# Kernel tuning notes

Hardware: AMD Instinct MI355X
Metric: run time of the kernel (lower is better)

Reference implementation:

```python
import jax, jax.numpy as jnp
import numpy as np

B, NL, NH = 16, 4096, 1024
CL, CH = 128, 256
IN_CH, OUT_CH = CH + CL, 256  # 384 -> 256
BN_EPS = 1e-5
K = 3


def setup_inputs() -> dict:
    key = jax.random.key(0)
    ks = jax.random.split(key, 8)
    xyz_low = jax.random.normal(ks[0], (B, NL, 3), jnp.float32)
    xyz_high = jax.random.normal(ks[1], (B, NH, 3), jnp.float32)
    feat_low = jax.random.normal(ks[2], (B, CL, NL), jnp.float32)
    feat_high = jax.random.normal(ks[3], (B, CH, NH), jnp.float32)
    # Conv1d(kernel=1) params, kaiming-ish scale
    W = jax.random.normal(ks[4], (OUT_CH, IN_CH), jnp.float32) * (1.0 / np.sqrt(IN_CH))
    b = jax.random.normal(ks[5], (OUT_CH,), jnp.float32) * 0.01
    gamma = jnp.ones((OUT_CH,), jnp.float32)
    beta = jnp.zeros((OUT_CH,), jnp.float32)
    return {"xyz_low": xyz_low, "xyz_high": xyz_high, "feat_low": feat_low,
            "feat_high": feat_high, "W": W, "b": b, "gamma": gamma, "beta": beta}


def reference(xyz_low, xyz_high, feat_low, feat_high, W, b, gamma, beta):
    # --- three_nn: pairwise Euclidean distances (B, Nl, Nh), as torch.cdist ---
    sq_l = jnp.sum(xyz_low * xyz_low, axis=-1)            # (B, Nl)
    sq_h = jnp.sum(xyz_high * xyz_high, axis=-1)          # (B, Nh)
    inner = jnp.einsum('bld,bhd->blh', xyz_low, xyz_high)  # (B, Nl, Nh)
    dist = jnp.sqrt(jnp.clip(sq_l[:, :, None] + sq_h[:, None, :] - 2.0 * inner, 0.0))
    # top-3 smallest distances
    neg_d3, idx = jax.lax.top_k(-dist, K)                 # idx: (B, Nl, 3)
    d3 = jnp.maximum(-neg_d3, 1e-8)                        # clamp_min(1e-8)
    w = 1.0 / d3
    w = w / jnp.sum(w, axis=-1, keepdims=True)             # (B, Nl, 3)
    # --- three_interpolate: gather neighbor features and weight ---
    fh = jnp.transpose(feat_high, (0, 2, 1))               # (B, Nh, Ch)
    neigh = jax.vmap(lambda f, i: f[i])(fh, idx)           # (B, Nl, 3, Ch)
    f_interp = jnp.einsum('blk,blkc->bcl', w, neigh)       # (B, Ch, Nl)
    f_cat = jnp.concatenate([f_interp, feat_low], axis=1)  # (B, in_ch, Nl)
    # --- Conv1d(k=1) + BatchNorm1d (training-mode batch stats) + ReLU ---
    y = jnp.einsum('oc,bcn->bon', W, f_cat) + b[None, :, None]
    mean = jnp.mean(y, axis=(0, 2), keepdims=True)
    var = jnp.mean((y - mean) ** 2, axis=(0, 2), keepdims=True)  # biased var
    y_hat = (y - mean) * jax.lax.rsqrt(var + BN_EPS)
    return jax.nn.relu(y_hat * gamma[None, :, None] + beta[None, :, None])
```

## Files before the change

kernel.cpp:

```cpp
#include <hip/hip_runtime.h>
#include <math.h>

constexpr int kB   = 16;
constexpr int kNL  = 4096;
constexpr int kNH  = 1024;
constexpr int kCL  = 128;
constexpr int kCH  = 256;
constexpr int kOUT = 256;

typedef __attribute__((ext_vector_type(8))) short s16x8;
typedef __attribute__((ext_vector_type(8))) unsigned short u16x8;
typedef __attribute__((ext_vector_type(4))) unsigned short u16x4;
typedef __attribute__((ext_vector_type(4))) float f32x4;

__device__ __forceinline__ unsigned short f2bf(float x) {
    unsigned int u = __float_as_uint(x);
    return (unsigned short)((u + 0x7FFFu + ((u >> 16) & 1u)) >> 16);
}
__device__ __forceinline__ unsigned int f2bf_pk(float a, float b) {
    return (unsigned int)f2bf(a) | ((unsigned int)f2bf(b) << 16);
}
__device__ __forceinline__ float bf2f(unsigned short h) {
    return __uint_as_float((unsigned int)h << 16);
}

__global__ void k_prep_w(const float* __restrict__ W, unsigned short* __restrict__ w1,
                         unsigned short* __restrict__ w2) {
    int o = blockIdx.x, k = threadIdx.x;
    float v = W[o * 384 + k];
    if (k < kCH) w1[o * kCH + k] = f2bf(v);
    else         w2[o * kCL + (k - kCH)] = f2bf(v);
}

__global__ void k_prep_cand(const float* __restrict__ xyzh, float4* __restrict__ cand) {
    int b = blockIdx.x;
    const float* H = xyzh + (size_t)b * kNH * 3;
    for (int j = threadIdx.x; j < kNH; j += 256) {
        float xx = H[j * 3 + 0], yy = H[j * 3 + 1], zz = H[j * 3 + 2];
        float s = __fmul_rn(xx, xx);
        s = __fadd_rn(s, __fmul_rn(yy, yy));
        s = __fadd_rn(s, __fmul_rn(zz, zz));
        cand[(size_t)b * kNH + j] = make_float4(xx + xx, yy + yy, zz + zz, s);
    }
}

__global__ __launch_bounds__(512) void k_three_nn(
    const float* __restrict__ xyzl, const float4* __restrict__ cand,
    float* __restrict__ w3, int* __restrict__ idx3)
{
    __shared__ float md[64][8][3];
    __shared__ int   midx[64][8][3];
    int b = blockIdx.y, t = threadIdx.x;
    int sub = t >> 6, ll = t & 63;
    int l = blockIdx.x * 64 + ll;

    const float* L = xyzl + ((size_t)b * kNL + l) * 3;
    float x = L[0], y = L[1], z = L[2];
    float sql = __fmul_rn(x, x);
    sql = __fadd_rn(sql, __fmul_rn(y, y));
    sql = __fadd_rn(sql, __fmul_rn(z, z));

    float dA0 = 1e30f, dA1 = 1e30f, dA2 = 1e30f;
    int   iA0 = 0,     iA1 = 0,     iA2 = 0;
    float dB0 = 1e30f, dB1 = 1e30f, dB2 = 1e30f;
    int   iB0 = 0,     iB1 = 0,     iB2 = 0;

    int jbeg = __builtin_amdgcn_readfirstlane(sub << 7);
    const float4* C = cand + ((size_t)b << 10) + jbeg;

    #pragma unroll 4
    for (int jj = 0; jj < 64; ++jj) {
        {
            float4 c = C[jj];
            float inner2 = __fmul_rn(x, c.x);
            inner2 = __fadd_rn(inner2, __fmul_rn(y, c.y));
            inner2 = __fadd_rn(inner2, __fmul_rn(z, c.z));
            float dsq = __fsub_rn(__fadd_rn(sql, c.w), inner2);
            dsq = fmaxf(dsq, 0.0f);
            int j = jbeg + jj;
            bool c0 = dsq < dA0, c1 = dsq < dA1, c2 = dsq < dA2;
            float td = c1 ? dA1 : dsq;  int ti = c1 ? iA1 : j;
            dA2 = c2 ? td : dA2;        iA2 = c2 ? ti : iA2;
            td = c0 ? dA0 : dsq;        ti = c0 ? iA0 : j;
            dA1 = c1 ? td : dA1;        iA1 = c1 ? ti : iA1;
            dA0 = c0 ? dsq : dA0;       iA0 = c0 ? j : iA0;
        }
        {
            float4 c = C[64 + jj];
            float inner2 = __fmul_rn(x, c.x);
            inner2 = __fadd_rn(inner2, __fmul_rn(y, c.y));
            inner2 = __fadd_rn(inner2, __fmul_rn(z, c.z));
            float dsq = __fsub_rn(__fadd_rn(sql, c.w), inner2);
            dsq = fmaxf(dsq, 0.0f);
            int j = jbeg + 64 + jj;
            bool c0 = dsq < dB0, c1 = dsq < dB1, c2 = dsq < dB2;
            float td = c1 ? dB1 : dsq;  int ti = c1 ? iB1 : j;
            dB2 = c2 ? td : dB2;        iB2 = c2 ? ti : iB2;
            td = c0 ? dB0 : dsq;        ti = c0 ? iB0 : j;
            dB1 = c1 ? td : dB1;        iB1 = c1 ? ti : iB1;
            dB0 = c0 ? dsq : dB0;       iB0 = c0 ? j : iB0;
        }
    }

    #pragma unroll
    for (int m = 0; m < 3; ++m) {
        float d = (m == 0) ? dB0 : (m == 1) ? dB1 : dB2;
        int  ii = (m == 0) ? iB0 : (m == 1) ? iB1 : iB2;
        bool lt2 = (d < dA2) || (d == dA2 && ii < iA2);
        if (lt2) {
            bool lt0 = (d < dA0) || (d == dA0 && ii < iA0);
            bool lt1 = (d < dA1) || (d == dA1 && ii < iA1);
            if (lt0)      { dA2 = dA1; iA2 = iA1; dA1 = dA0; iA1 = iA0; dA0 = d; iA0 = ii; }
            else if (lt1) { dA2 = dA1; iA2 = iA1; dA1 = d; iA1 = ii; }
            else          { dA2 = d; iA2 = ii; }
        }
    }

    md[ll][sub][0] = dA0;  md[ll][sub][1] = dA1;  md[ll][sub][2] = dA2;
    midx[ll][sub][0] = iA0; midx[ll][sub][1] = iA1; midx[ll][sub][2] = iA2;
    __syncthreads();

    if (sub == 0) {
        float e0 = 1e30f, e1 = 1e30f, e2 = 1e30f;
        int   a0 = 0x7fffffff, a1 = 0x7fffffff, a2 = 0x7fffffff;
        #pragma unroll
        for (int s = 0; s < 8; ++s) {
            #pragma unroll
            for (int k = 0; k < 3; ++k) {
                float d = md[ll][s][k]; int ii = midx[ll][s][k];
                bool lt2 = (d < e2) || (d == e2 && ii < a2);
                if (lt2) {
                    bool lt0 = (d < e0) || (d == e0 && ii < a0);
                    bool lt1 = (d < e1) || (d == e1 && ii < a1);
                    if (lt0)      { e2 = e1; a2 = a1; e1 = e0; a1 = a0; e0 = d; a0 = ii; }
                    else if (lt1) { e2 = e1; a2 = a1; e1 = d; a1 = ii; }
                    else          { e2 = d; a2 = ii; }
                }
            }
        }
        float q0 = fmaxf(sqrtf(e0), 1e-8f);
        float q1 = fmaxf(sqrtf(e1), 1e-8f);
        float q2 = fmaxf(sqrtf(e2), 1e-8f);
        float r0 = 1.0f / q0, r1 = 1.0f / q1, r2 = 1.0f / q2;
        float s = __fadd_rn(__fadd_rn(r0, r1), r2);
        size_t base = ((size_t)b * kNL + l) * 3;
        w3[base + 0] = r0 / s;  w3[base + 1] = r1 / s;  w3[base + 2] = r2 / s;
        idx3[base + 0] = a0;    idx3[base + 1] = a1;    idx3[base + 2] = a2;
    }
}

__global__ __launch_bounds__(256, 4) void k_gemm1(
    const float* __restrict__ fhigh, const unsigned short* __restrict__ w1,
    unsigned short* __restrict__ gtb)
{
    __shared__ __align__(16) unsigned short Bt[64][264];
    int b = blockIdx.y, j0 = blockIdx.x * 64, t = threadIdx.x;
    const float* src = fhigh + (size_t)b * kCH * kNH + j0;
    #pragma unroll
    for (int i = 0; i < 8; ++i) {
        int e = t + i * 256, cp = e >> 4, j4 = e & 15;
        f32x4 a  = *(const f32x4*)(src + (size_t)(2 * cp)     * kNH + 4 * j4);
        f32x4 b2 = *(const f32x4*)(src + (size_t)(2 * cp + 1) * kNH + 4 * j4);
        #pragma unroll
        for (int r = 0; r < 4; ++r)
            *(unsigned int*)(&Bt[4 * j4 + r][2 * cp]) = f2bf_pk(a[r], b2[r]);
    }
    __syncthreads();

    int w = t >> 6, lane = t & 63, lo = lane & 15, hi = lane >> 4;
    f32x4 vz = {0.f, 0.f, 0.f, 0.f};
    f32x4 acc[4][4];
    #pragma unroll
    for (int mi = 0; mi < 4; ++mi)
        #pragma unroll
        for (int ni = 0; ni < 4; ++ni) acc[mi][ni] = vz;

    #pragma unroll
    for (int ks = 0; ks < 8; ++ks) {
        s16x8 av[4], bv[4];
        #pragma unroll
        for (int mi = 0; mi < 4; ++mi)
            av[mi] = *(const s16x8*)(w1 + (size_t)(64 * w + 16 * mi + lo) * kCH + ks * 32 + hi * 8);
        #pragma unroll
        for (int ni = 0; ni < 4; ++ni)
            bv[ni] = *(const s16x8*)(&Bt[16 * ni + lo][ks * 32 + hi * 8]);
        #pragma unroll
        for (int mi = 0; mi < 4; ++mi)
            #pragma unroll
            for (int ni = 0; ni < 4; ++ni)
                acc[mi][ni] = __builtin_amdgcn_mfma_f32_16x16x32_bf16(av[mi], bv[ni], acc[mi][ni], 0, 0, 0);
    }

    unsigned short* G = gtb + ((size_t)b * kNH + j0) * kOUT;
    #pragma unroll
    for (int mi = 0; mi < 4; ++mi)
        #pragma unroll
        for (int ni = 0; ni < 4; ++ni) {
            f32x4 a = acc[mi][ni];
            u16x4 h;
            #pragma unroll
            for (int r = 0; r < 4; ++r) h[r] = f2bf(a[r]);
            *(u16x4*)(&G[(size_t)(16 * ni + lo) * kOUT + w * 64 + hi * 16 + mi * 4]) = h;
        }
}

__global__ __launch_bounds__(256, 4) void k_gemm2(
    const float* __restrict__ flow, const unsigned short* __restrict__ w2,
    const unsigned short* __restrict__ gtb, const float* __restrict__ bias,
    const float* __restrict__ w3, const int* __restrict__ idx3,
    unsigned short* __restrict__ ybf, float* __restrict__ ps, float* __restrict__ pq)
{
    __shared__ __align__(16) char smem[17408];
    unsigned short (*Bt)[136] = (unsigned short (*)[136])smem;
    float* red = (float*)smem;
    __shared__ float wc[64][3];
    __shared__ int   ic[64][3];

    int b = blockIdx.y, n0 = blockIdx.x * 64, t = threadIdx.x;
    int blin = b * gridDim.x + blockIdx.x;

    if (t < 192) {
        int n = t / 3, k = t - n * 3;
        wc[n][k] = w3[((size_t)b * kNL + n0 + n) * 3 + k];
        ic[n][k] = idx3[((size_t)b * kNL + n0 + n) * 3 + k];
    }
    const float* src = flow + (size_t)b * kCL * kNL + n0;
    #pragma unroll
    for (int i = 0; i < 4; ++i) {
        int e = t + i * 256, cp = e >> 4, n4 = e & 15;
        f32x4 a  = *(const f32x4*)(src + (size_t)(2 * cp)     * kNL + 4 * n4);
        f32x4 b2 = *(const f32x4*)(src + (size_t)(2 * cp + 1) * kNL + 4 * n4);
        #pragma unroll
        for (int r = 0; r < 4; ++r)
            *(unsigned int*)(&Bt[4 * n4 + r][2 * cp]) = f2bf_pk(a[r], b2[r]);
    }
    __syncthreads();

    int w = t >> 6, lane = t & 63, lo = lane & 15, hi = lane >> 4;
    f32x4 vz = {0.f, 0.f, 0.f, 0.f};
    f32x4 acc[4][4];
    #pragma unroll
    for (int mi = 0; mi < 4; ++mi)
        #pragma unroll
        for (int ni = 0; ni < 4; ++ni) acc[mi][ni] = vz;

    #pragma unroll
    for (int ks = 0; ks < 4; ++ks) {
        s16x8 av[4], bv[4];
        #pragma unroll
        for (int mi = 0; mi < 4; ++mi)
            av[mi] = *(const s16x8*)(w2 + (size_t)(64 * w + 16 * mi + lo) * kCL + ks * 32 + hi * 8);
        #pragma unroll
        for (int ni = 0; ni < 4; ++ni)
            bv[ni] = *(const s16x8*)(&Bt[16 * ni + lo][ks * 32 + hi * 8]);
        #pragma unroll
        for (int mi = 0; mi < 4; ++mi)
            #pragma unroll
            for (int ni = 0; ni < 4; ++ni)
                acc[mi][ni] = __builtin_amdgcn_mfma_f32_16x16x32_bf16(av[mi], bv[ni], acc[mi][ni], 0, 0, 0);
    }

    const unsigned short* Gb = gtb + (size_t)b * kNH * kOUT + w * 64 + hi * 16;
    #pragma unroll
    for (int k = 0; k < 3; ++k) {
        u16x8 g0[4], g1[4];
        float wcr[4];
        #pragma unroll
        for (int ni = 0; ni < 4; ++ni) {
            int lc = 16 * ni + lo;
            int jj = ic[lc][k];
            wcr[ni] = wc[lc][k];
            const u16x8* p = (const u16x8*)(Gb + (size_t)jj * kOUT);
            g0[ni] = p[0];
            g1[ni] = p[1];
        }
        #pragma unroll
        for (int ni = 0; ni < 4; ++ni) {
            float wg = wcr[ni];
            #pragma unroll
            for (int r = 0; r < 4; ++r) {
                acc[0][ni][r] = fmaf(wg, bf2f(g0[ni][r]),     acc[0][ni][r]);
                acc[1][ni][r] = fmaf(wg, bf2f(g0[ni][4 + r]), acc[1][ni][r]);
                acc[2][ni][r] = fmaf(wg, bf2f(g1[ni][r]),     acc[2][ni][r]);
                acc[3][ni][r] = fmaf(wg, bf2f(g1[ni][4 + r]), acc[3][ni][r]);
            }
        }
    }
    #pragma unroll
    for (int mi = 0; mi < 4; ++mi) {
        f32x4 bb = *(const f32x4*)(bias + 64 * w + 16 * mi + 4 * hi);
        #pragma unroll
        for (int ni = 0; ni < 4; ++ni) acc[mi][ni] += bb;
    }

    unsigned short* Y = ybf + (size_t)b * kOUT * kNL + n0;
    #pragma unroll
    for (int mi = 0; mi < 4; ++mi)
        #pragma unroll
        for (int ni = 0; ni < 4; ++ni)
            #pragma unroll
            for (int r = 0; r < 4; ++r)
                Y[(size_t)(64 * w + 16 * mi + 4 * hi + r) * kNL + 16 * ni + lo] = f2bf(acc[mi][ni][r]);

    int ow = t >> 6, omi = (t >> 4) & 3, ohi = (t >> 2) & 3, orr = t & 3;
    __syncthreads();
    #pragma unroll
    for (int mi = 0; mi < 4; ++mi) {
        f32x4 s = acc[mi][0] + acc[mi][1] + acc[mi][2] + acc[mi][3];
        #pragma unroll
        for (int r = 0; r < 4; ++r) red[t * 17 + mi * 4 + r] = s[r];
    }
    __syncthreads();
    float ssum = 0.0f;
    #pragma unroll
    for (int l2 = 0; l2 < 16; ++l2)
        ssum += red[(ow * 64 + ohi * 16 + l2) * 17 + omi * 4 + orr];
    __syncthreads();
    #pragma unroll
    for (int mi = 0; mi < 4; ++mi) {
        f32x4 q = acc[mi][0] * acc[mi][0] + acc[mi][1] * acc[mi][1]
                + acc[mi][2] * acc[mi][2] + acc[mi][3] * acc[mi][3];
        #pragma unroll
        for (int r = 0; r < 4; ++r) red[t * 17 + mi * 4 + r] = q[r];
    }
    __syncthreads();
    float qsum = 0.0f;
    #pragma unroll
    for (int l2 = 0; l2 < 16; ++l2)
        qsum += red[(ow * 64 + ohi * 16 + l2) * 17 + omi * 4 + orr];

    ps[(size_t)t * 1024 + blin] = ssum;
    pq[(size_t)t * 1024 + blin] = qsum;
}

__global__ void k_finalize(const float* __restrict__ ps, const float* __restrict__ pq,
                           const float* __restrict__ gamma, const float* __restrict__ beta,
                           float* __restrict__ cA, float* __restrict__ cB) {
    int o = blockIdx.x, t = threadIdx.x;
    float s = 0.0f, q = 0.0f;
    #pragma unroll
    for (int i = 0; i < 4; ++i) {
        s += ps[(size_t)o * 1024 + t + i * 256];
        q += pq[(size_t)o * 1024 + t + i * 256];
    }
    #pragma unroll
    for (int off = 32; off > 0; off >>= 1) {
        s += __shfl_down(s, off);
        q += __shfl_down(q, off);
    }
    __shared__ float ls[4], lq[4];
    if ((t & 63) == 0) { ls[t >> 6] = s; lq[t >> 6] = q; }
    __syncthreads();
    if (t == 0) {
        s = ls[0] + ls[1] + ls[2] + ls[3];
        q = lq[0] + lq[1] + lq[2] + lq[3];
        const float inv = 1.0f / (float)(kB * kNL);
        float mean = s * inv;
        float var  = q * inv - mean * mean;
        float a = gamma[o] * rsqrtf(var + 1e-5f);
        cA[o] = a;
        cB[o] = beta[o] - mean * a;
    }
}

__global__ void k_apply(const unsigned short* __restrict__ ybf, float* __restrict__ out,
                        const float* __restrict__ cA, const float* __restrict__ cB) {
    size_t idx    = (size_t)blockIdx.x * 256 + threadIdx.x;
    size_t stride = (size_t)gridDim.x * 256;
    const size_t n8 = (size_t)kB * kOUT * kNL / 8;
    const u16x8* yp = (const u16x8*)ybf;
    float4* op = (float4*)out;
    for (size_t i = idx; i < n8; i += stride) {
        int o = (int)((i >> 9) & 255);
        float a = cA[o], c = cB[o];
        u16x8 v = yp[i];
        float4 r0, r1;
        r0.x = fmaxf(fmaf(a, bf2f(v[0]), c), 0.0f);
        r0.y = fmaxf(fmaf(a, bf2f(v[1]), c), 0.0f);
        r0.z = fmaxf(fmaf(a, bf2f(v[2]), c), 0.0f);
        r0.w = fmaxf(fmaf(a, bf2f(v[3]), c), 0.0f);
        r1.x = fmaxf(fmaf(a, bf2f(v[4]), c), 0.0f);
        r1.y = fmaxf(fmaf(a, bf2f(v[5]), c), 0.0f);
        r1.z = fmaxf(fmaf(a, bf2f(v[6]), c), 0.0f);
        r1.w = fmaxf(fmaf(a, bf2f(v[7]), c), 0.0f);
        op[2 * i]     = r0;
        op[2 * i + 1] = r1;
    }
}

extern "C" void kernel_launch(void* const* d_in, const int* in_sizes, int n_in,
                              void* d_out, int out_size, void* d_ws, size_t ws_size,
                              hipStream_t stream) {
    const float* xyzl  = (const float*)d_in[0];
    const float* xyzh  = (const float*)d_in[1];
    const float* flow  = (const float*)d_in[2];
    const float* fhigh = (const float*)d_in[3];
    const float* W     = (const float*)d_in[4];
    const float* bias  = (const float*)d_in[5];
    const float* gamma = (const float*)d_in[6];
    const float* beta  = (const float*)d_in[7];
    float* out = (float*)d_out;
    char*  ws  = (char*)d_ws;
    (void)in_sizes; (void)n_in; (void)out_size; (void)ws_size;

    float*          w3   = (float*)(ws + 0);
    int*            idx3 = (int*)  (ws + 786432);
    unsigned short* gtb  = (unsigned short*)(ws + 1572864);
    unsigned short* ybf  = (unsigned short*)(ws + 9961472);
    unsigned short* w1   = (unsigned short*)(ws + 43515904);
    unsigned short* w2   = (unsigned short*)(ws + 43646976);
    float*          ps   = (float*)(ws + 43712512);
    float*          pq   = (float*)(ws + 44761088);
    float*          cA   = (float*)(ws + 45809664);
    float*          cB   = (float*)(ws + 45810688);
    float4*         cand = (float4*)(ws + 45811712);

    hipLaunchKernelGGL(k_prep_w,    dim3(256),          dim3(384), 0, stream, W, w1, w2);
    hipLaunchKernelGGL(k_prep_cand, dim3(kB),           dim3(256), 0, stream, xyzh, cand);
    hipLaunchKernelGGL(k_three_nn,  dim3(kNL / 64, kB), dim3(512), 0, stream, xyzl, cand, w3, idx3);
    hipLaunchKernelGGL(k_gemm1,     dim3(kNH / 64, kB), dim3(256), 0, stream, fhigh, w1, gtb);
    hipLaunchKernelGGL(k_gemm2,     dim3(kNL / 64, kB), dim3(256), 0, stream,
                       flow, w2, gtb, bias, w3, idx3, ybf, ps, pq);
    hipLaunchKernelGGL(k_finalize,  dim3(256),          dim3(256), 0, stream, ps, pq, gamma, beta, cA, cB);
    hipLaunchKernelGGL(k_apply,     dim3(2048),         dim3(256), 0, stream, ybf, out, cA, cB);
}
```

Baseline: 121.9 us.

## Fuse three-NN search into gemm2 and alternate its order with MFMA loop

```diff
diff --git a/kernel.cpp b/kernel.cpp
--- a/kernel.cpp
+++ b/kernel.cpp
@@ -44,111 +44,6 @@
     }
 }
 
-__global__ __launch_bounds__(512) void k_three_nn(
-    const float* __restrict__ xyzl, const float4* __restrict__ cand,
-    float* __restrict__ w3, int* __restrict__ idx3)
-{
-    __shared__ float md[64][8][3];
-    __shared__ int   midx[64][8][3];
-    int b = blockIdx.y, t = threadIdx.x;
-    int sub = t >> 6, ll = t & 63;
-    int l = blockIdx.x * 64 + ll;
-
-    const float* L = xyzl + ((size_t)b * kNL + l) * 3;
-    float x = L[0], y = L[1], z = L[2];
-    float sql = __fmul_rn(x, x);
-    sql = __fadd_rn(sql, __fmul_rn(y, y));
-    sql = __fadd_rn(sql, __fmul_rn(z, z));
-
-    float dA0 = 1e30f, dA1 = 1e30f, dA2 = 1e30f;
-    int   iA0 = 0,     iA1 = 0,     iA2 = 0;
-    float dB0 = 1e30f, dB1 = 1e30f, dB2 = 1e30f;
-    int   iB0 = 0,     iB1 = 0,     iB2 = 0;
-
-    int jbeg = __builtin_amdgcn_readfirstlane(sub << 7);
-    const float4* C = cand + ((size_t)b << 10) + jbeg;
-
-    #pragma unroll 4
-    for (int jj = 0; jj < 64; ++jj) {
-        {
-            float4 c = C[jj];
-            float inner2 = __fmul_rn(x, c.x);
-            inner2 = __fadd_rn(inner2, __fmul_rn(y, c.y));
-            inner2 = __fadd_rn(inner2, __fmul_rn(z, c.z));
-            float dsq = __fsub_rn(__fadd_rn(sql, c.w), inner2);
-            dsq = fmaxf(dsq, 0.0f);
-            int j = jbeg + jj;
-            bool c0 = dsq < dA0, c1 = dsq < dA1, c2 = dsq < dA2;
-            float td = c1 ? dA1 : dsq;  int ti = c1 ? iA1 : j;
-            dA2 = c2 ? td : dA2;        iA2 = c2 ? ti : iA2;
-            td = c0 ? dA0 : dsq;        ti = c0 ? iA0 : j;
-            dA1 = c1 ? td : dA1;        iA1 = c1 ? ti : iA1;
-            dA0 = c0 ? dsq : dA0;       iA0 = c0 ? j : iA0;
-        }
-        {
-            float4 c = C[64 + jj];
-            float inner2 = __fmul_rn(x, c.x);
-            inner2 = __fadd_rn(inner2, __fmul_rn(y, c.y));
-            inner2 = __fadd_rn(inner2, __fmul_rn(z, c.z));
-            float dsq = __fsub_rn(__fadd_rn(sql, c.w), inner2);
-            dsq = fmaxf(dsq, 0.0f);
-            int j = jbeg + 64 + jj;
-            bool c0 = dsq < dB0, c1 = dsq < dB1, c2 = dsq < dB2;
-            float td = c1 ? dB1 : dsq;  int ti = c1 ? iB1 : j;
-            dB2 = c2 ? td : dB2;        iB2 = c2 ? ti : iB2;
-            td = c0 ? dB0 : dsq;        ti = c0 ? iB0 : j;
-            dB1 = c1 ? td : dB1;        iB1 = c1 ? ti : iB1;
-            dB0 = c0 ? dsq : dB0;       iB0 = c0 ? j : iB0;
-        }
-    }
-
-    #pragma unroll
-    for (int m = 0; m < 3; ++m) {
-        float d = (m == 0) ? dB0 : (m == 1) ? dB1 : dB2;
-        int  ii = (m == 0) ? iB0 : (m == 1) ? iB1 : iB2;
-        bool lt2 = (d < dA2) || (d == dA2 && ii < iA2);
-        if (lt2) {
-            bool lt0 = (d < dA0) || (d == dA0 && ii < iA0);
-            bool lt1 = (d < dA1) || (d == dA1 && ii < iA1);
-            if (lt0)      { dA2 = dA1; iA2 = iA1; dA1 = dA0; iA1 = iA0; dA0 = d; iA0 = ii; }
-            else if (lt1) { dA2 = dA1; iA2 = iA1; dA1 = d; iA1 = ii; }
-            else          { dA2 = d; iA2 = ii; }
-        }
-    }
-
-    md[ll][sub][0] = dA0;  md[ll][sub][1] = dA1;  md[ll][sub][2] = dA2;
-    midx[ll][sub][0] = iA0; midx[ll][sub][1] = iA1; midx[ll][sub][2] = iA2;
-    __syncthreads();
-
-    if (sub == 0) {
-        float e0 = 1e30f, e1 = 1e30f, e2 = 1e30f;
-        int   a0 = 0x7fffffff, a1 = 0x7fffffff, a2 = 0x7fffffff;
-        #pragma unroll
-        for (int s = 0; s < 8; ++s) {
-            #pragma unroll
-            for (int k = 0; k < 3; ++k) {
-                float d = md[ll][s][k]; int ii = midx[ll][s][k];
-                bool lt2 = (d < e2) || (d == e2 && ii < a2);
-                if (lt2) {
-                    bool lt0 = (d < e0) || (d == e0 && ii < a0);
-                    bool lt1 = (d < e1) || (d == e1 && ii < a1);
-                    if (lt0)      { e2 = e1; a2 = a1; e1 = e0; a1 = a0; e0 = d; a0 = ii; }
-                    else if (lt1) { e2 = e1; a2 = a1; e1 = d; a1 = ii; }
-                    else          { e2 = d; a2 = ii; }
-                }
-            }
-        }
-        float q0 = fmaxf(sqrtf(e0), 1e-8f);
-        float q1 = fmaxf(sqrtf(e1), 1e-8f);
-        float q2 = fmaxf(sqrtf(e2), 1e-8f);
-        float r0 = 1.0f / q0, r1 = 1.0f / q1, r2 = 1.0f / q2;
-        float s = __fadd_rn(__fadd_rn(r0, r1), r2);
-        size_t base = ((size_t)b * kNL + l) * 3;
-        w3[base + 0] = r0 / s;  w3[base + 1] = r1 / s;  w3[base + 2] = r2 / s;
-        idx3[base + 0] = a0;    idx3[base + 1] = a1;    idx3[base + 2] = a2;
-    }
-}
-
 __global__ __launch_bounds__(256, 4) void k_gemm1(
     const float* __restrict__ fhigh, const unsigned short* __restrict__ w1,
     unsigned short* __restrict__ gtb)
@@ -207,7 +102,7 @@
 __global__ __launch_bounds__(256, 4) void k_gemm2(
     const float* __restrict__ flow, const unsigned short* __restrict__ w2,
     const unsigned short* __restrict__ gtb, const float* __restrict__ bias,
-    const float* __restrict__ w3, const int* __restrict__ idx3,
+    const float* __restrict__ xyzl, const float4* __restrict__ cand,
     unsigned short* __restrict__ ybf, float* __restrict__ ps, float* __restrict__ pq)
 {
     __shared__ __align__(16) char smem[17408];
@@ -215,15 +110,12 @@
     float* red = (float*)smem;
     __shared__ float wc[64][3];
     __shared__ int   ic[64][3];
+    __shared__ float md[64][4][3];
+    __shared__ int   midx[64][4][3];
 
     int b = blockIdx.y, n0 = blockIdx.x * 64, t = threadIdx.x;
     int blin = b * gridDim.x + blockIdx.x;
 
-    if (t < 192) {
-        int n = t / 3, k = t - n * 3;
-        wc[n][k] = w3[((size_t)b * kNL + n0 + n) * 3 + k];
-        ic[n][k] = idx3[((size_t)b * kNL + n0 + n) * 3 + k];
-    }
     const float* src = flow + (size_t)b * kCL * kNL + n0;
     #pragma unroll
     for (int i = 0; i < 4; ++i) {
@@ -244,21 +136,124 @@
         #pragma unroll
         for (int ni = 0; ni < 4; ++ni) acc[mi][ni] = vz;
 
-    #pragma unroll
-    for (int ks = 0; ks < 4; ++ks) {
-        s16x8 av[4], bv[4];
-        #pragma unroll
-        for (int mi = 0; mi < 4; ++mi)
-            av[mi] = *(const s16x8*)(w2 + (size_t)(64 * w + 16 * mi + lo) * kCL + ks * 32 + hi * 8);
-        #pragma unroll
-        for (int ni = 0; ni < 4; ++ni)
-            bv[ni] = *(const s16x8*)(&Bt[16 * ni + lo][ks * 32 + hi * 8]);
-        #pragma unroll
-        for (int mi = 0; mi < 4; ++mi)
+    auto do_nn = [&]() {
+        int sub = t >> 6, ll = t & 63;
+        int l = n0 + ll;
+        const float* L = xyzl + ((size_t)b * kNL + l) * 3;
+        float x = L[0], y = L[1], z = L[2];
+        float sql = __fmul_rn(x, x);
+        sql = __fadd_rn(sql, __fmul_rn(y, y));
+        sql = __fadd_rn(sql, __fmul_rn(z, z));
+
+        float dA0 = 1e30f, dA1 = 1e30f, dA2 = 1e30f;
+        int   iA0 = 0,     iA1 = 0,     iA2 = 0;
+        float dB0 = 1e30f, dB1 = 1e30f, dB2 = 1e30f;
+        int   iB0 = 0,     iB1 = 0,     iB2 = 0;
+
+        int jbeg = __builtin_amdgcn_readfirstlane(sub << 8);
+        const float4* C = cand + ((size_t)b << 10) + jbeg;
+
+        #pragma unroll 4
+        for (int jj = 0; jj < 128; ++jj) {
+            {
+                float4 c = C[jj];
+                float inner2 = __fmul_rn(x, c.x);
+                inner2 = __fadd_rn(inner2, __fmul_rn(y, c.y));
+                inner2 = __fadd_rn(inner2, __fmul_rn(z, c.z));
+                float dsq = __fsub_rn(__fadd_rn(sql, c.w), inner2);
+                dsq = fmaxf(dsq, 0.0f);
+                int j = jbeg + jj;
+                bool c0 = dsq < dA0, c1 = dsq < dA1, c2 = dsq < dA2;
+                float td = c1 ? dA1 : dsq;  int ti = c1 ? iA1 : j;
+                dA2 = c2 ? td : dA2;        iA2 = c2 ? ti : iA2;
+                td = c0 ? dA0 : dsq;        ti = c0 ? iA0 : j;
+                dA1 = c1 ? td : dA1;        iA1 = c1 ? ti : iA1;
+                dA0 = c0 ? dsq : dA0;       iA0 = c0 ? j : iA0;
+            }
+            {
+                float4 c = C[128 + jj];
+                float inner2 = __fmul_rn(x, c.x);
+                inner2 = __fadd_rn(inner2, __fmul_rn(y, c.y));
+                inner2 = __fadd_rn(inner2, __fmul_rn(z, c.z));
+                float dsq = __fsub_rn(__fadd_rn(sql, c.w), inner2);
+                dsq = fmaxf(dsq, 0.0f);
+                int j = jbeg + 128 + jj;
+                bool c0 = dsq < dB0, c1 = dsq < dB1, c2 = dsq < dB2;
+                float td = c1 ? dB1 : dsq;  int ti = c1 ? iB1 : j;
+                dB2 = c2 ? td : dB2;        iB2 = c2 ? ti : iB2;
+                td = c0 ? dB0 : dsq;        ti = c0 ? iB0 : j;
+                dB1 = c1 ? td : dB1;        iB1 = c1 ? ti : iB1;
+                dB0 = c0 ? dsq : dB0;       iB0 = c0 ? j : iB0;
+            }
+        }
+
+        #pragma unroll
+        for (int m = 0; m < 3; ++m) {
+            float d = (m == 0) ? dB0 : (m == 1) ? dB1 : dB2;
+            int  ii = (m == 0) ? iB0 : (m == 1) ? iB1 : iB2;
+            bool lt2 = (d < dA2) || (d == dA2 && ii < iA2);
+            if (lt2) {
+                bool lt0 = (d < dA0) || (d == dA0 && ii < iA0);
+                bool lt1 = (d < dA1) || (d == dA1 && ii < iA1);
+                if (lt0)      { dA2 = dA1; iA2 = iA1; dA1 = dA0; iA1 = iA0; dA0 = d; iA0 = ii; }
+                else if (lt1) { dA2 = dA1; iA2 = iA1; dA1 = d; iA1 = ii; }
+                else          { dA2 = d; iA2 = ii; }
+            }
+        }
+
+        md[ll][sub][0] = dA0;  md[ll][sub][1] = dA1;  md[ll][sub][2] = dA2;
+        midx[ll][sub][0] = iA0; midx[ll][sub][1] = iA1; midx[ll][sub][2] = iA2;
+        __syncthreads();
+
+        if (sub == 0) {
+            float e0 = 1e30f, e1 = 1e30f, e2 = 1e30f;
+            int   a0 = 0x7fffffff, a1 = 0x7fffffff, a2 = 0x7fffffff;
+            #pragma unroll
+            for (int s = 0; s < 4; ++s) {
+                #pragma unroll
+                for (int k = 0; k < 3; ++k) {
+                    float d = md[ll][s][k]; int ii = midx[ll][s][k];
+                    bool lt2 = (d < e2) || (d == e2 && ii < a2);
+                    if (lt2) {
+                        bool lt0 = (d < e0) || (d == e0 && ii < a0);
+                        bool lt1 = (d < e1) || (d == e1 && ii < a1);
+                        if (lt0)      { e2 = e1; a2 = a1; e1 = e0; a1 = a0; e0 = d; a0 = ii; }
+                        else if (lt1) { e2 = e1; a2 = a1; e1 = d; a1 = ii; }
+                        else          { e2 = d; a2 = ii; }
+                    }
+                }
+            }
+            float q0 = fmaxf(sqrtf(e0), 1e-8f);
+            float q1 = fmaxf(sqrtf(e1), 1e-8f);
+            float q2 = fmaxf(sqrtf(e2), 1e-8f);
+            float r0 = 1.0f / q0, r1 = 1.0f / q1, r2 = 1.0f / q2;
+            float s = __fadd_rn(__fadd_rn(r0, r1), r2);
+            wc[ll][0] = r0 / s;  wc[ll][1] = r1 / s;  wc[ll][2] = r2 / s;
+            ic[ll][0] = a0;      ic[ll][1] = a1;      ic[ll][2] = a2;
+        }
+    };
+
+    auto do_kloop = [&]() {
+        #pragma unroll
+        for (int ks = 0; ks < 4; ++ks) {
+            s16x8 av[4], bv[4];
+            #pragma unroll
+            for (int mi = 0; mi < 4; ++mi)
+                av[mi] = *(const s16x8*)(w2 + (size_t)(64 * w + 16 * mi + lo) * kCL + ks * 32 + hi * 8);
             #pragma unroll
             for (int ni = 0; ni < 4; ++ni)
-                acc[mi][ni] = __builtin_amdgcn_mfma_f32_16x16x32_bf16(av[mi], bv[ni], acc[mi][ni], 0, 0, 0);
-    }
+                bv[ni] = *(const s16x8*)(&Bt[16 * ni + lo][ks * 32 + hi * 8]);
+            #pragma unroll
+            for (int mi = 0; mi < 4; ++mi)
+                #pragma unroll
+                for (int ni = 0; ni < 4; ++ni)
+                    acc[mi][ni] = __builtin_amdgcn_mfma_f32_16x16x32_bf16(av[mi], bv[ni], acc[mi][ni], 0, 0, 0);
+        }
+    };
+
+    if (blockIdx.x & 1) { do_kloop(); do_nn(); }
+    else                { do_nn();    do_kloop(); }
+    __syncthreads();
 
     const unsigned short* Gb = gtb + (size_t)b * kNH * kOUT + w * 64 + hi * 16;
     #pragma unroll
@@ -403,24 +398,21 @@
     char*  ws  = (char*)d_ws;
     (void)in_sizes; (void)n_in; (void)out_size; (void)ws_size;
 
-    float*          w3   = (float*)(ws + 0);
-    int*            idx3 = (int*)  (ws + 786432);
-    unsigned short* gtb  = (unsigned short*)(ws + 1572864);
-    unsigned short* ybf  = (unsigned short*)(ws + 9961472);
-    unsigned short* w1   = (unsigned short*)(ws + 43515904);
-    unsigned short* w2   = (unsigned short*)(ws + 43646976);
-    float*          ps   = (float*)(ws + 43712512);
-    float*          pq   = (float*)(ws + 44761088);
-    float*          cA   = (float*)(ws + 45809664);
-    float*          cB   = (float*)(ws + 45810688);
-    float4*         cand = (float4*)(ws + 45811712);
+    unsigned short* gtb  = (unsigned short*)(ws + 0);
+    unsigned short* ybf  = (unsigned short*)(ws + 8388608);
+    unsigned short* w1   = (unsigned short*)(ws + 41943040);
+    unsigned short* w2   = (unsigned short*)(ws + 42074112);
+    float*          ps   = (float*)(ws + 42139648);
+    float*          pq   = (float*)(ws + 43188224);
+    float*          cA   = (float*)(ws + 44236800);
+    float*          cB   = (float*)(ws + 44237824);
+    float4*         cand = (float4*)(ws + 44238848);
 
     hipLaunchKernelGGL(k_prep_w,    dim3(256),          dim3(384), 0, stream, W, w1, w2);
     hipLaunchKernelGGL(k_prep_cand, dim3(kB),           dim3(256), 0, stream, xyzh, cand);
-    hipLaunchKernelGGL(k_three_nn,  dim3(kNL / 64, kB), dim3(512), 0, stream, xyzl, cand, w3, idx3);
     hipLaunchKernelGGL(k_gemm1,     dim3(kNH / 64, kB), dim3(256), 0, stream, fhigh, w1, gtb);
     hipLaunchKernelGGL(k_gemm2,     dim3(kNL / 64, kB), dim3(256), 0, stream,
-                       flow, w2, gtb, bias, w3, idx3, ybf, ps, pq);
+                       flow, w2, gtb, bias, xyzl, cand, ybf, ps, pq);
     hipLaunchKernelGGL(k_finalize,  dim3(256),          dim3(256), 0, stream, ps, pq, gamma, beta, cA, cB);
     hipLaunchKernelGGL(k_apply,     dim3(2048),         dim3(256), 0, stream, ybf, out, cA, cB);
 }
```

Measured after the change: 104.2 us. -14.5%, faster.

## Merge three_nn and gemm1 into one heterogeneous kernel launch

Applied to the files above, without the earlier changes.

```diff
diff --git a/kernel.cpp b/kernel.cpp
--- a/kernel.cpp
+++ b/kernel.cpp
@@ -44,164 +44,170 @@
     }
 }
 
-__global__ __launch_bounds__(512) void k_three_nn(
+__global__ __launch_bounds__(256, 4) void k_mega(
+    const float* __restrict__ fhigh, const unsigned short* __restrict__ w1,
+    unsigned short* __restrict__ gtb,
     const float* __restrict__ xyzl, const float4* __restrict__ cand,
     float* __restrict__ w3, int* __restrict__ idx3)
 {
-    __shared__ float md[64][8][3];
-    __shared__ int   midx[64][8][3];
-    int b = blockIdx.y, t = threadIdx.x;
-    int sub = t >> 6, ll = t & 63;
-    int l = blockIdx.x * 64 + ll;
-
-    const float* L = xyzl + ((size_t)b * kNL + l) * 3;
-    float x = L[0], y = L[1], z = L[2];
-    float sql = __fmul_rn(x, x);
-    sql = __fadd_rn(sql, __fmul_rn(y, y));
-    sql = __fadd_rn(sql, __fmul_rn(z, z));
-
-    float dA0 = 1e30f, dA1 = 1e30f, dA2 = 1e30f;
-    int   iA0 = 0,     iA1 = 0,     iA2 = 0;
-    float dB0 = 1e30f, dB1 = 1e30f, dB2 = 1e30f;
-    int   iB0 = 0,     iB1 = 0,     iB2 = 0;
-
-    int jbeg = __builtin_amdgcn_readfirstlane(sub << 7);
-    const float4* C = cand + ((size_t)b << 10) + jbeg;
-
-    #pragma unroll 4
-    for (int jj = 0; jj < 64; ++jj) {
-        {
-            float4 c = C[jj];
-            float inner2 = __fmul_rn(x, c.x);
-            inner2 = __fadd_rn(inner2, __fmul_rn(y, c.y));
-            inner2 = __fadd_rn(inner2, __fmul_rn(z, c.z));
-            float dsq = __fsub_rn(__fadd_rn(sql, c.w), inner2);
-            dsq = fmaxf(dsq, 0.0f);
-            int j = jbeg + jj;
-            bool c0 = dsq < dA0, c1 = dsq < dA1, c2 = dsq < dA2;
-            float td = c1 ? dA1 : dsq;  int ti = c1 ? iA1 : j;
-            dA2 = c2 ? td : dA2;        iA2 = c2 ? ti : iA2;
-            td = c0 ? dA0 : dsq;        ti = c0 ? iA0 : j;
-            dA1 = c1 ? td : dA1;        iA1 = c1 ? ti : iA1;
-            dA0 = c0 ? dsq : dA0;       iA0 = c0 ? j : iA0;
-        }
-        {
-            float4 c = C[64 + jj];
-            float inner2 = __fmul_rn(x, c.x);
-            inner2 = __fadd_rn(inner2, __fmul_rn(y, c.y));
-            inner2 = __fadd_rn(inner2, __fmul_rn(z, c.z));
-            float dsq = __fsub_rn(__fadd_rn(sql, c.w), inner2);
-            dsq = fmaxf(dsq, 0.0f);
-            int j = jbeg + 64 + jj;
-            bool c0 = dsq < dB0, c1 = dsq < dB1, c2 = dsq < dB2;
-            float td = c1 ? dB1 : dsq;  int ti = c1 ? iB1 : j;
-            dB2 = c2 ? td : dB2;        iB2 = c2 ? ti : iB2;
-            td = c0 ? dB0 : dsq;        ti = c0 ? iB0 : j;
-            dB1 = c1 ? td : dB1;        iB1 = c1 ? ti : iB1;
-            dB0 = c0 ? dsq : dB0;       iB0 = c0 ? j : iB0;
-        }
-    }
-
-    #pragma unroll
-    for (int m = 0; m < 3; ++m) {
-        float d = (m == 0) ? dB0 : (m == 1) ? dB1 : dB2;
-        int  ii = (m == 0) ? iB0 : (m == 1) ? iB1 : iB2;
-        bool lt2 = (d < dA2) || (d == dA2 && ii < iA2);
-        if (lt2) {
-            bool lt0 = (d < dA0) || (d == dA0 && ii < iA0);
-            bool lt1 = (d < dA1) || (d == dA1 && ii < iA1);
-            if (lt0)      { dA2 = dA1; iA2 = iA1; dA1 = dA0; iA1 = iA0; dA0 = d; iA0 = ii; }
-            else if (lt1) { dA2 = dA1; iA2 = iA1; dA1 = d; iA1 = ii; }
-            else          { dA2 = d; iA2 = ii; }
-        }
-    }
-
-    md[ll][sub][0] = dA0;  md[ll][sub][1] = dA1;  md[ll][sub][2] = dA2;
-    midx[ll][sub][0] = iA0; midx[ll][sub][1] = iA1; midx[ll][sub][2] = iA2;
-    __syncthreads();
-
-    if (sub == 0) {
-        float e0 = 1e30f, e1 = 1e30f, e2 = 1e30f;
-        int   a0 = 0x7fffffff, a1 = 0x7fffffff, a2 = 0x7fffffff;
-        #pragma unroll
-        for (int s = 0; s < 8; ++s) {
-            #pragma unroll
-            for (int k = 0; k < 3; ++k) {
-                float d = md[ll][s][k]; int ii = midx[ll][s][k];
-                bool lt2 = (d < e2) || (d == e2 && ii < a2);
-                if (lt2) {
-                    bool lt0 = (d < e0) || (d == e0 && ii < a0);
-                    bool lt1 = (d < e1) || (d == e1 && ii < a1);
-                    if (lt0)      { e2 = e1; a2 = a1; e1 = e0; a1 = a0; e0 = d; a0 = ii; }
-                    else if (lt1) { e2 = e1; a2 = a1; e1 = d; a1 = ii; }
-                    else          { e2 = d; a2 = ii; }
+    __shared__ __align__(16) char smem[33792];
+    int bid = blockIdx.x, t = threadIdx.x;
+
+    if (bid % 5 == 0) {
+        unsigned short (*Bt)[264] = (unsigned short (*)[264])smem;
+        int g = bid / 5;
+        int b = g >> 4, j0 = (g & 15) * 64;
+        const float* src = fhigh + (size_t)b * kCH * kNH + j0;
+        #pragma unroll
+        for (int i = 0; i < 8; ++i) {
+            int e = t + i * 256, cp = e >> 4, j4 = e & 15;
+            f32x4 a  = *(const f32x4*)(src + (size_t)(2 * cp)     * kNH + 4 * j4);
+            f32x4 b2 = *(const f32x4*)(src + (size_t)(2 * cp + 1) * kNH + 4 * j4);
+            #pragma unroll
+            for (int r = 0; r < 4; ++r)
+                *(unsigned int*)(&Bt[4 * j4 + r][2 * cp]) = f2bf_pk(a[r], b2[r]);
+        }
+        __syncthreads();
+
+        int w = t >> 6, lane = t & 63, lo = lane & 15, hi = lane >> 4;
+        f32x4 vz = {0.f, 0.f, 0.f, 0.f};
+        f32x4 acc[4][4];
+        #pragma unroll
+        for (int mi = 0; mi < 4; ++mi)
+            #pragma unroll
+            for (int ni = 0; ni < 4; ++ni) acc[mi][ni] = vz;
+
+        #pragma unroll
+        for (int ks = 0; ks < 8; ++ks) {
+            s16x8 av[4], bv[4];
+            #pragma unroll
+            for (int mi = 0; mi < 4; ++mi)
+                av[mi] = *(const s16x8*)(w1 + (size_t)(64 * w + 16 * mi + lo) * kCH + ks * 32 + hi * 8);
+            #pragma unroll
+            for (int ni = 0; ni < 4; ++ni)
+                bv[ni] = *(const s16x8*)(&Bt[16 * ni + lo][ks * 32 + hi * 8]);
+            #pragma unroll
+            for (int mi = 0; mi < 4; ++mi)
+                #pragma unroll
+                for (int ni = 0; ni < 4; ++ni)
+                    acc[mi][ni] = __builtin_amdgcn_mfma_f32_16x16x32_bf16(av[mi], bv[ni], acc[mi][ni], 0, 0, 0);
+        }
+
+        unsigned short* G = gtb + ((size_t)b * kNH + j0) * kOUT;
+        #pragma unroll
+        for (int mi = 0; mi < 4; ++mi)
+            #pragma unroll
+            for (int ni = 0; ni < 4; ++ni) {
+                f32x4 a = acc[mi][ni];
+                u16x4 h;
+                #pragma unroll
+                for (int r = 0; r < 4; ++r) h[r] = f2bf(a[r]);
+                *(u16x4*)(&G[(size_t)(16 * ni + lo) * kOUT + w * 64 + hi * 16 + mi * 4]) = h;
+            }
+    } else {
+        float* md  = (float*)smem;
+        int*   mip = (int*)(smem + 3072);
+        int s = bid - bid / 5 - 1;
+        int b = s >> 6, n0 = (s & 63) * 64;
+        int sub = t >> 6, ll = t & 63;
+        int l = n0 + ll;
+
+        const float* L = xyzl + ((size_t)b * kNL + l) * 3;
+        float x = L[0], y = L[1], z = L[2];
+        float sql = __fmul_rn(x, x);
+        sql = __fadd_rn(sql, __fmul_rn(y, y));
+        sql = __fadd_rn(sql, __fmul_rn(z, z));
+
+        float dA0 = 1e30f, dA1 = 1e30f, dA2 = 1e30f;
+        int   iA0 = 0,     iA1 = 0,     iA2 = 0;
+        float dB0 = 1e30f, dB1 = 1e30f, dB2 = 1e30f;
+        int   iB0 = 0,     iB1 = 0,     iB2 = 0;
+
+        int jbeg = __builtin_amdgcn_readfirstlane(sub << 8);
+        const float4* C = cand + ((size_t)b << 10) + jbeg;
+
+        #pragma unroll 4
+        for (int jj = 0; jj < 128; ++jj) {
+            {
+                float4 c = C[jj];
+                float inner2 = __fmul_rn(x, c.x);
+                inner2 = __fadd_rn(inner2, __fmul_rn(y, c.y));
+                inner2 = __fadd_rn(inner2, __fmul_rn(z, c.z));
+                float dsq = __fsub_rn(__fadd_rn(sql, c.w), inner2);
+                dsq = fmaxf(dsq, 0.0f);
+                int j = jbeg + jj;
+                bool c0 = dsq < dA0, c1 = dsq < dA1, c2 = dsq < dA2;
+                float td = c1 ? dA1 : dsq;  int ti = c1 ? iA1 : j;
+                dA2 = c2 ? td : dA2;        iA2 = c2 ? ti : iA2;
+                td = c0 ? dA0 : dsq;        ti = c0 ? iA0 : j;
+                dA1 = c1 ? td : dA1;        iA1 = c1 ? ti : iA1;
+                dA0 = c0 ? dsq : dA0;       iA0 = c0 ? j : iA0;
+            }
+            {
+                float4 c = C[128 + jj];
+                float inner2 = __fmul_rn(x, c.x);
+                inner2 = __fadd_rn(inner2, __fmul_rn(y, c.y));
+                inner2 = __fadd_rn(inner2, __fmul_rn(z, c.z));
+                float dsq = __fsub_rn(__fadd_rn(sql, c.w), inner2);
+                dsq = fmaxf(dsq, 0.0f);
+                int j = jbeg + 128 + jj;
+                bool c0 = dsq < dB0, c1 = dsq < dB1, c2 = dsq < dB2;
+                float td = c1 ? dB1 : dsq;  int ti = c1 ? iB1 : j;
+                dB2 = c2 ? td : dB2;        iB2 = c2 ? ti : iB2;
+                td = c0 ? dB0 : dsq;        ti = c0 ? iB0 : j;
+                dB1 = c1 ? td : dB1;        iB1 = c1 ? ti : iB1;
+                dB0 = c0 ? dsq : dB0;       iB0 = c0 ? j : iB0;
+            }
+        }
+
+        #pragma unroll
+        for (int m = 0; m < 3; ++m) {
+            float d = (m == 0) ? dB0 : (m == 1) ? dB1 : dB2;
+            int  ii = (m == 0) ? iB0 : (m == 1) ? iB1 : iB2;
+            bool lt2 = (d < dA2) || (d == dA2 && ii < iA2);
+            if (lt2) {
+                bool lt0 = (d < dA0) || (d == dA0 && ii < iA0);
+                bool lt1 = (d < dA1) || (d == dA1 && ii < iA1);
+                if (lt0)      { dA2 = dA1; iA2 = iA1; dA1 = dA0; iA1 = iA0; dA0 = d; iA0 = ii; }
+                else if (lt1) { dA2 = dA1; iA2 = iA1; dA1 = d; iA1 = ii; }
+                else          { dA2 = d; iA2 = ii; }
+            }
+        }
+
+        int mo = (ll * 4 + sub) * 3;
+        md[mo + 0] = dA0;  md[mo + 1] = dA1;  md[mo + 2] = dA2;
+        mip[mo + 0] = iA0; mip[mo + 1] = iA1; mip[mo + 2] = iA2;
+        __syncthreads();
+
+        if (sub == 0) {
+            float e0 = 1e30f, e1 = 1e30f, e2 = 1e30f;
+            int   a0 = 0x7fffffff, a1 = 0x7fffffff, a2 = 0x7fffffff;
+            #pragma unroll
+            for (int ss = 0; ss < 4; ++ss) {
+                #pragma unroll
+                for (int k = 0; k < 3; ++k) {
+                    float d = md[(ll * 4 + ss) * 3 + k];
+                    int  ii = mip[(ll * 4 + ss) * 3 + k];
+                    bool lt2 = (d < e2) || (d == e2 && ii < a2);
+                    if (lt2) {
+                        bool lt0 = (d < e0) || (d == e0 && ii < a0);
+                        bool lt1 = (d < e1) || (d == e1 && ii < a1);
+                        if (lt0)      { e2 = e1; a2 = a1; e1 = e0; a1 = a0; e0 = d; a0 = ii; }
+                        else if (lt1) { e2 = e1; a2 = a1; e1 = d; a1 = ii; }
+                        else          { e2 = d; a2 = ii; }
+                    }
                 }
             }
-        }
-        float q0 = fmaxf(sqrtf(e0), 1e-8f);
-        float q1 = fmaxf(sqrtf(e1), 1e-8f);
-        float q2 = fmaxf(sqrtf(e2), 1e-8f);
-        float r0 = 1.0f / q0, r1 = 1.0f / q1, r2 = 1.0f / q2;
-        float s = __fadd_rn(__fadd_rn(r0, r1), r2);
-        size_t base = ((size_t)b * kNL + l) * 3;
-        w3[base + 0] = r0 / s;  w3[base + 1] = r1 / s;  w3[base + 2] = r2 / s;
-        idx3[base + 0] = a0;    idx3[base + 1] = a1;    idx3[base + 2] = a2;
-    }
-}
-
-__global__ __launch_bounds__(256, 4) void k_gemm1(
-    const float* __restrict__ fhigh, const unsigned short* __restrict__ w1,
-    unsigned short* __restrict__ gtb)
-{
-    __shared__ __align__(16) unsigned short Bt[64][264];
-    int b = blockIdx.y, j0 = blockIdx.x * 64, t = threadIdx.x;
-    const float* src = fhigh + (size_t)b * kCH * kNH + j0;
-    #pragma unroll
-    for (int i = 0; i < 8; ++i) {
-        int e = t + i * 256, cp = e >> 4, j4 = e & 15;
-        f32x4 a  = *(const f32x4*)(src + (size_t)(2 * cp)     * kNH + 4 * j4);
-        f32x4 b2 = *(const f32x4*)(src + (size_t)(2 * cp + 1) * kNH + 4 * j4);
-        #pragma unroll
-        for (int r = 0; r < 4; ++r)
-            *(unsigned int*)(&Bt[4 * j4 + r][2 * cp]) = f2bf_pk(a[r], b2[r]);
-    }
-    __syncthreads();
-
-    int w = t >> 6, lane = t & 63, lo = lane & 15, hi = lane >> 4;
-    f32x4 vz = {0.f, 0.f, 0.f, 0.f};
-    f32x4 acc[4][4];
-    #pragma unroll
-    for (int mi = 0; mi < 4; ++mi)
-        #pragma unroll
-        for (int ni = 0; ni < 4; ++ni) acc[mi][ni] = vz;
-
-    #pragma unroll
-    for (int ks = 0; ks < 8; ++ks) {
-        s16x8 av[4], bv[4];
-        #pragma unroll
-        for (int mi = 0; mi < 4; ++mi)
-            av[mi] = *(const s16x8*)(w1 + (size_t)(64 * w + 16 * mi + lo) * kCH + ks * 32 + hi * 8);
-        #pragma unroll
-        for (int ni = 0; ni < 4; ++ni)
-            bv[ni] = *(const s16x8*)(&Bt[16 * ni + lo][ks * 32 + hi * 8]);
-        #pragma unroll
-        for (int mi = 0; mi < 4; ++mi)
-            #pragma unroll
-            for (int ni = 0; ni < 4; ++ni)
-                acc[mi][ni] = __builtin_amdgcn_mfma_f32_16x16x32_bf16(av[mi], bv[ni], acc[mi][ni], 0, 0, 0);
-    }
-
-    unsigned short* G = gtb + ((size_t)b * kNH + j0) * kOUT;
-    #pragma unroll
-    for (int mi = 0; mi < 4; ++mi)
-        #pragma unroll
-        for (int ni = 0; ni < 4; ++ni) {
-            f32x4 a = acc[mi][ni];
-            u16x4 h;
-            #pragma unroll
-            for (int r = 0; r < 4; ++r) h[r] = f2bf(a[r]);
-            *(u16x4*)(&G[(size_t)(16 * ni + lo) * kOUT + w * 64 + hi * 16 + mi * 4]) = h;
-        }
+            float q0 = fmaxf(sqrtf(e0), 1e-8f);
+            float q1 = fmaxf(sqrtf(e1), 1e-8f);
+            float q2 = fmaxf(sqrtf(e2), 1e-8f);
+            float r0 = 1.0f / q0, r1 = 1.0f / q1, r2 = 1.0f / q2;
+            float sw = __fadd_rn(__fadd_rn(r0, r1), r2);
+            size_t base = ((size_t)b * kNL + l) * 3;
+            w3[base + 0] = r0 / sw;  w3[base + 1] = r1 / sw;  w3[base + 2] = r2 / sw;
+            idx3[base + 0] = a0;     idx3[base + 1] = a1;     idx3[base + 2] = a2;
+        }
+    }
 }
 
 __global__ __launch_bounds__(256, 4) void k_gemm2(
@@ -417,8 +423,8 @@
 
     hipLaunchKernelGGL(k_prep_w,    dim3(256),          dim3(384), 0, stream, W, w1, w2);
     hipLaunchKernelGGL(k_prep_cand, dim3(kB),           dim3(256), 0, stream, xyzh, cand);
-    hipLaunchKernelGGL(k_three_nn,  dim3(kNL / 64, kB), dim3(512), 0, stream, xyzl, cand, w3, idx3);
-    hipLaunchKernelGGL(k_gemm1,     dim3(kNH / 64, kB), dim3(256), 0, stream, fhigh, w1, gtb);
+    hipLaunchKernelGGL(k_mega,      dim3(1280),         dim3(256), 0, stream,
+                       fhigh, w1, gtb, xyzl, cand, w3, idx3);
     hipLaunchKernelGGL(k_gemm2,     dim3(kNL / 64, kB), dim3(256), 0, stream,
                        flow, w2, gtb, bias, w3, idx3, ybf, ps, pq);
     hipLaunchKernelGGL(k_finalize,  dim3(256),          dim3(256), 0, stream, ps, pq, gamma, beta, cA, cB);
```

Result: no change. 121.7 us (-0.2%).
